# Kernel optimization log

Hardware: AMD Instinct MI355X
Metric: run time of the kernel (lower is better)

The kernel has to match this reference:

```python
import jax, jax.numpy as jnp
import numpy as np

D_MODEL, D_STATE, D_CONV, EXPAND = 1024, 16, 4, 2
D_INNER = EXPAND * D_MODEL
DT_RANK = max(16, D_MODEL // 16)
B_SZ, T_LEN = 2, 2048


def setup_inputs() -> dict:
    key = jax.random.key(0)
    ks = jax.random.split(key, 12)
    s = lambda fan: 1.0 / np.sqrt(fan)
    x = jax.random.normal(ks[0], (B_SZ, T_LEN, D_MODEL), jnp.float32)
    sigma2 = jax.random.uniform(ks[1], (B_SZ, T_LEN, 1), jnp.float32)
    W_in = jax.random.normal(ks[2], (D_MODEL, 2 * D_INNER), jnp.float32) * s(D_MODEL)
    conv_w = jax.random.normal(ks[3], (D_CONV, 1, D_INNER), jnp.float32) * s(D_CONV)
    conv_b = jax.random.normal(ks[4], (D_INNER,), jnp.float32) * 0.01
    W_xproj = jax.random.normal(ks[5], (D_INNER, 2 * D_STATE + DT_RANK), jnp.float32) * s(D_INNER)
    W_delta = jax.random.normal(ks[6], (D_MODEL, D_INNER), jnp.float32) * s(D_MODEL)
    b_delta = jax.random.normal(ks[7], (D_INNER,), jnp.float32) * 0.01
    A_log = jnp.log(jnp.tile(jnp.arange(1, D_STATE + 1, dtype=jnp.float32), (D_INNER, 1)))
    D_param = jnp.ones((D_INNER,), jnp.float32)
    W_out = jax.random.normal(ks[8], (D_INNER, D_MODEL), jnp.float32) * s(D_INNER)
    alpha = jnp.float32(1.0)
    return {"x": x, "sigma2": sigma2, "W_in": W_in, "conv_w": conv_w, "conv_b": conv_b,
            "W_xproj": W_xproj, "W_delta": W_delta, "b_delta": b_delta, "A_log": A_log,
            "D_param": D_param, "W_out": W_out, "alpha": alpha}


def _forward(x, sigma2, W_in, conv_w, conv_b, W_xproj, W_delta, b_delta, A_log, D_param, W_out, alpha):
    # in_proj and split
    xz = jnp.einsum('btd,de->bte', x, W_in)
    u, z = jnp.split(xz, 2, axis=-1)                      # (B,T,d_inner) each
    # causal depthwise conv1d (left pad d_conv-1, truncate to T)
    u = jax.lax.conv_general_dilated(
        u, conv_w, window_strides=(1,), padding=[(D_CONV - 1, 0)],
        dimension_numbers=('NHC', 'HIO', 'NHC'), feature_group_count=D_INNER) + conv_b
    u = jax.nn.silu(u)
    # x_proj -> B, C (delta_raw_proj branch is unused in custom-delta path)
    x_dbl = jnp.einsum('bti,ij->btj', u, W_xproj)
    Bp = x_dbl[..., :D_STATE]                              # (B,T,d_state)
    Cp = x_dbl[..., D_STATE:2 * D_STATE]                   # (B,T,d_state)
    # quality-gated custom delta
    delta_raw = jax.nn.softplus(jnp.einsum('btd,di->bti', x, W_delta) + b_delta)
    delta = delta_raw * jnp.exp(-alpha * sigma2)           # (B,T,d_inner)
    A = -jnp.exp(A_log)                                    # (d_inner,d_state)
    # discretize
    dA = jnp.exp(delta[..., None] * A)                     # (B,T,d_inner,d_state)
    dBu = delta[..., None] * Bp[:, :, None, :] * u[..., None]

    def step(h, inp):
        dA_t, dBu_t, c_t = inp                             # (B,di,ds),(B,di,ds),(B,ds)
        h = dA_t * h + dBu_t
        y_t = jnp.sum(h * c_t[:, None, :], axis=-1)        # (B,d_inner)
        return h, y_t

    h0 = jnp.zeros((x.shape[0], D_INNER, D_STATE), dtype=u.dtype)
    _, ys = jax.lax.scan(step, h0, (jnp.moveaxis(dA, 1, 0), jnp.moveaxis(dBu, 1, 0), jnp.moveaxis(Cp, 1, 0)))
    y = jnp.moveaxis(ys, 0, 1) + u * D_param               # (B,T,d_inner)
    y = y * jax.nn.silu(z)
    return jnp.einsum('bti,id->btd', y, W_out)


def reference(x, sigma2, W_in, conv_w, conv_b, W_xproj, W_delta, b_delta, A_log, D_param, W_out, alpha):
    return _forward(x, sigma2, W_in, conv_w, conv_b, W_xproj, W_delta, b_delta, A_log, D_param, W_out, alpha)
```

## Files before the change

### kernel.cpp

```cpp
#include <hip/hip_runtime.h>
#include <math.h>


constexpr int D_MODEL = 1024;
constexpr int D_STATE = 16;
constexpr int D_CONV  = 4;
constexpr int D_INNER = 2048;
constexpr int XPROJ_W = 96;
constexpr int B_SZ = 2, T_LEN = 2048;
constexpr int ROWS = B_SZ * T_LEN;
constexpr int NCHUNK = 64, CHUNK = T_LEN / NCHUNK;

typedef unsigned short ushort_t;
typedef __bf16 bf16x8 __attribute__((ext_vector_type(8)));
typedef float f32x4 __attribute__((ext_vector_type(4)));

__device__ __forceinline__ ushort_t f2bf(float f) {
  unsigned int u = __float_as_uint(f);
  u = (u + 0x7fffu + ((u >> 16) & 1u)) >> 16;
  return (ushort_t)u;
}
__device__ __forceinline__ float bf2f(ushort_t h) {
  return __uint_as_float(((unsigned int)h) << 16);
}

__device__ __forceinline__ void gload16(const void* g, void* l) {
  __builtin_amdgcn_global_load_lds(
      (const __attribute__((address_space(1))) void*)g,
      (__attribute__((address_space(3))) void*)l, 16, 0, 0);
}

__global__ __launch_bounds__(256)
void convert_all_kernel(const float* __restrict__ x,
                        const float* __restrict__ W_in,
                        const float* __restrict__ W_delta,
                        const float* __restrict__ W_out,
                        ushort_t* __restrict__ xb, ushort_t* __restrict__ WiT,
                        ushort_t* __restrict__ WdT, ushort_t* __restrict__ WoT)
{
  __shared__ float tile[32][33];
  const int blk = blockIdx.x;
  const int tid = threadIdx.x;
  if (blk < 4096) {
    const int i = blk * 256 + tid;
    const float4 v = ((const float4*)x)[i];
    ushort_t tmp[4] = {f2bf(v.x), f2bf(v.y), f2bf(v.z), f2bf(v.w)};
    ((uint2*)xb)[i] = *(const uint2*)tmp;
    return;
  }
  const float* in;
  ushort_t* out;
  int R, C, t;
  if (blk < 8192)      { in = W_in;    out = WiT; R = 1024; C = 4096; t = blk - 4096;  }
  else if (blk < 10240){ in = W_delta; out = WdT; R = 1024; C = 2048; t = blk - 8192;  }
  else                 { in = W_out;   out = WoT; R = 2048; C = 1024; t = blk - 10240; }
  const int tpr = C / 32;
  const int c0 = (t % tpr) * 32, r0 = (t / tpr) * 32;
  const int tx = tid & 31, ty = tid >> 5;
#pragma unroll
  for (int i = 0; i < 32; i += 8)
    tile[ty + i][tx] = in[(size_t)(r0 + ty + i) * C + c0 + tx];
  __syncthreads();
#pragma unroll
  for (int i = 0; i < 32; i += 8)
    out[(size_t)(c0 + ty + i) * R + r0 + tx] = f2bf(tile[tx][ty + i]);
}

template <int MODE, int BM>
__global__ __launch_bounds__(256)
void gemm_t(const ushort_t* __restrict__ A, const ushort_t* __restrict__ Bt,
            const int lda, const int ldb, const int KT,
            ushort_t* __restrict__ outB, float* __restrict__ outF,
            const float* __restrict__ bias, const float* __restrict__ sigma2,
            const float* __restrict__ alphap)
{
  constexpr int MREP = (BM == 32) ? 2 : 4;
  constexpr int NREP = (BM == 128) ? 4 : 2;
  constexpr int RT = BM + 128;
  constexpr int CH = RT / 32;

  __shared__ __align__(16) ushort_t As[BM * 64];
  __shared__ __align__(16) ushort_t Bs[128 * 64];
  const int tid = threadIdx.x;
  const int wave = tid >> 6, lane = tid & 63;
  const int lc = lane & 15, lr = lane >> 4;
  const int m0 = blockIdx.y * BM, n0 = blockIdx.x * 128;
  const int N = gridDim.x * 128;
  const int arow = (BM == 128) ? ((wave >> 1) * 64) : 0;
  const int bcol = (BM == 128) ? ((wave & 1) * 64) : (wave * 32);

  f32x4 acc[MREP][NREP];
#pragma unroll
  for (int i = 0; i < MREP; ++i)
#pragma unroll
    for (int j = 0; j < NREP; ++j) acc[i][j] = (f32x4)0.f;

  const int rlane = lane >> 3;
  const int clane = (lane & 7) * 8;

  for (int kt = 0; kt < KT; ++kt) {
    if (kt) __syncthreads();
    const int k0 = kt * 64;
#pragma unroll
    for (int i = 0; i < CH; ++i) {
      const int r0c = (wave * CH + i) * 8;
      if (r0c < BM) {
        gload16(A + (size_t)(m0 + r0c + rlane) * lda + k0 + clane,
                &As[r0c * 64]);
      } else {
        const int br = r0c - BM;
        gload16(Bt + (size_t)(n0 + br + rlane) * ldb + k0 + clane,
                &Bs[br * 64]);
      }
    }
    __syncthreads();
#pragma unroll
    for (int ks = 0; ks < 2; ++ks) {
      bf16x8 af[MREP], bfr[NREP];
#pragma unroll
      for (int mi = 0; mi < MREP; ++mi)
        af[mi] = *(const bf16x8*)
            &As[(arow + mi * 16 + lc) * 64 + ks * 32 + lr * 8];
#pragma unroll
      for (int ni = 0; ni < NREP; ++ni)
        bfr[ni] = *(const bf16x8*)
            &Bs[(bcol + ni * 16 + lc) * 64 + ks * 32 + lr * 8];
#pragma unroll
      for (int mi = 0; mi < MREP; ++mi)
#pragma unroll
        for (int ni = 0; ni < NREP; ++ni)
          acc[mi][ni] = __builtin_amdgcn_mfma_f32_16x16x32_bf16(
              af[mi], bfr[ni], acc[mi][ni], 0, 0, 0);
    }
  }

  const float alphaV = (MODE == 2) ? alphap[0] : 0.f;
#pragma unroll
  for (int mi = 0; mi < MREP; ++mi) {
    const int rowb = m0 + arow + mi * 16 + lr * 4;
#pragma unroll
    for (int ni = 0; ni < NREP; ++ni) {
      const int col = n0 + bcol + ni * 16 + lc;
      f32x4 v = acc[mi][ni];
      if (MODE == 0) {
#pragma unroll
        for (int r = 0; r < 4; ++r)
          outB[(size_t)(rowb + r) * N + col] = f2bf(v[r]);
      } else if (MODE == 2) {
        const float bv = bias[col];
#pragma unroll
        for (int r = 0; r < 4; ++r) {
          const float xv = v[r] + bv;
          const float sp = (xv > 20.f) ? xv : log1pf(__expf(xv));
          outB[(size_t)(rowb + r) * N + col] =
              f2bf(sp * __expf(-alphaV * sigma2[rowb + r]));
        }
      } else {
#pragma unroll
        for (int r = 0; r < 4; ++r)
          outF[(size_t)(rowb + r) * N + col] = v[r];
      }
    }
  }
}

__device__ __forceinline__ void decay_powers(float d, float (&dA)[16])
{
  const float q1 = __expf(-d);
  const float q2 = q1 * q1, q3 = q2 * q1, q4 = q2 * q2;
  const float q8 = q4 * q4, q12 = q8 * q4;
  dA[0] = q1;        dA[1] = q2;        dA[2] = q3;        dA[3] = q4;
  dA[4] = q4 * q1;   dA[5] = q4 * q2;   dA[6] = q4 * q3;   dA[7] = q8;
  dA[8] = q8 * q1;   dA[9] = q8 * q2;   dA[10] = q8 * q3;  dA[11] = q12;
  dA[12] = q12 * q1; dA[13] = q12 * q2; dA[14] = q12 * q3; dA[15] = q12 * q4;
}

__global__ __launch_bounds__(256)
void conv_xproj_kernel(const ushort_t* __restrict__ xzb,
                       const float* __restrict__ cw,
                       const float* __restrict__ cb,
                       const float* __restrict__ Wx,
                       ushort_t* __restrict__ u, float* __restrict__ BC)
{
  __shared__ float us[8][D_INNER];
  __shared__ float red[8][8][32];
  const int tid = threadIdx.x;
  const int b = blockIdx.y;
  const int t0 = blockIdx.x * 8;
  const int ch0 = tid * 8;

  float wtk[4][8], bs[8];
#pragma unroll
  for (int k = 0; k < 4; ++k) {
    float4 wa = *(const float4*)&cw[k * D_INNER + ch0];
    float4 wb = *(const float4*)&cw[k * D_INNER + ch0 + 4];
    wtk[k][0] = wa.x; wtk[k][1] = wa.y; wtk[k][2] = wa.z; wtk[k][3] = wa.w;
    wtk[k][4] = wb.x; wtk[k][5] = wb.y; wtk[k][6] = wb.z; wtk[k][7] = wb.w;
  }
  {
    float4 ba = *(const float4*)&cb[ch0];
    float4 bb = *(const float4*)&cb[ch0 + 4];
    bs[0] = ba.x; bs[1] = ba.y; bs[2] = ba.z; bs[3] = ba.w;
    bs[4] = bb.x; bs[5] = bb.y; bs[6] = bb.z; bs[7] = bb.w;
  }

#pragma unroll
  for (int r = 0; r < 8; ++r) {
    const int t = t0 + r;
    float acc[8];
#pragma unroll
    for (int j = 0; j < 8; ++j) acc[j] = bs[j];
#pragma unroll
    for (int k = 0; k < 4; ++k) {
      const int tt = t + k - 3;
      if (tt >= 0) {
        uint4 raw = *(const uint4*)
            &xzb[(size_t)(b * T_LEN + tt) * (2 * D_INNER) + ch0];
        const ushort_t* hp = (const ushort_t*)&raw;
#pragma unroll
        for (int j = 0; j < 8; ++j)
          acc[j] = fmaf(bf2f(hp[j]), wtk[k][j], acc[j]);
      }
    }
    ushort_t ub[8];
#pragma unroll
    for (int j = 0; j < 8; ++j) {
      const float ss = acc[j] / (1.f + __expf(-acc[j]));
      us[r][ch0 + j] = ss;
      ub[j] = f2bf(ss);
    }
    *(uint4*)&u[(size_t)(b * T_LEN + t) * D_INNER + ch0] = *(const uint4*)ub;
  }
  __syncthreads();

  const int j = tid & 31, chunk = tid >> 5;
  float p[8] = {0.f, 0.f, 0.f, 0.f, 0.f, 0.f, 0.f, 0.f};
  const float* WxC = Wx + j;
  for (int i = 0; i < 256; ++i) {
    const int k = chunk * 256 + i;
    const float w = WxC[(size_t)k * XPROJ_W];
#pragma unroll
    for (int r = 0; r < 8; ++r) p[r] = fmaf(us[r][k], w, p[r]);
  }
#pragma unroll
  for (int r = 0; r < 8; ++r) red[r][chunk][j] = p[r];
  __syncthreads();
  {
    const int r = tid >> 5, jj = tid & 31;
    float ssum = 0.f;
#pragma unroll
    for (int c = 0; c < 8; ++c) ssum += red[r][c][jj];
    BC[(size_t)(b * T_LEN + t0 + r) * 32 + jj] = ssum;
  }
}

__global__ __launch_bounds__(256)
void scan1_kernel(const ushort_t* __restrict__ delta,
                  const ushort_t* __restrict__ u,
                  const float* __restrict__ BC,
                  float* __restrict__ hEnd, float* __restrict__ sumD)
{
  const int c = blockIdx.x * 256 + threadIdx.x;
  const int b = blockIdx.y;
  const int j = blockIdx.z;
  float h[D_STATE];
#pragma unroll
  for (int n = 0; n < D_STATE; ++n) h[n] = 0.f;
  float sd = 0.f;
  const int t0 = j * CHUNK;
  for (int t = t0; t < t0 + CHUNK; ++t) {
    const int row = b * T_LEN + t;
    const float d = bf2f(delta[(size_t)row * D_INNER + c]);
    const float uu = bf2f(u[(size_t)row * D_INNER + c]);
    sd += d;
    const float du = d * uu;
    float dA[16];
    decay_powers(d, dA);
    const float4* bp4 = (const float4*)&BC[(size_t)row * 32];
    float4 b0 = bp4[0], b1 = bp4[1], b2 = bp4[2], b3 = bp4[3];
    const float bp[16] = {b0.x, b0.y, b0.z, b0.w, b1.x, b1.y, b1.z, b1.w,
                          b2.x, b2.y, b2.z, b2.w, b3.x, b3.y, b3.z, b3.w};
#pragma unroll
    for (int n = 0; n < D_STATE; ++n)
      h[n] = fmaf(dA[n], h[n], du * bp[n]);
  }
  const size_t base = ((size_t)b * D_INNER + c) * NCHUNK + j;
#pragma unroll
  for (int n = 0; n < D_STATE; ++n) hEnd[base * 16 + n] = h[n];
  sumD[base] = sd;
}

__global__ __launch_bounds__(256)
void scan2_kernel(float* __restrict__ hEnd, const float* __restrict__ sumD)
{
  const int idx = blockIdx.x * 256 + threadIdx.x;
  const int n = idx & 15;
  const int c = (idx >> 4) & (D_INNER - 1);
  const int b = idx >> 15;
  const float an = -(float)(n + 1);
  float H = 0.f;
  for (int j = 0; j < NCHUNK; ++j) {
    const size_t base = ((size_t)b * D_INNER + c) * NCHUNK + j;
    const float he = hEnd[base * 16 + n];
    const float sd = sumD[base];
    hEnd[base * 16 + n] = H;
    H = fmaf(__expf(an * sd), H, he);
  }
}

__global__ __launch_bounds__(256)
void scan3_kernel(const ushort_t* __restrict__ delta,
                  const ushort_t* __restrict__ u,
                  const float* __restrict__ BC,
                  const float* __restrict__ hStart,
                  const ushort_t* __restrict__ xzb,
                  const float* __restrict__ Dp, ushort_t* __restrict__ yb)
{
  const int c = blockIdx.x * 256 + threadIdx.x;
  const int b = blockIdx.y;
  const int j = blockIdx.z;
  float h[D_STATE];
  const size_t base = ((size_t)b * D_INNER + c) * NCHUNK + j;
#pragma unroll
  for (int n = 0; n < D_STATE; ++n) h[n] = hStart[base * 16 + n];
  const float dpc = Dp[c];
  const int t0 = j * CHUNK;
  for (int t = t0; t < t0 + CHUNK; ++t) {
    const int row = b * T_LEN + t;
    const float d = bf2f(delta[(size_t)row * D_INNER + c]);
    const float uu = bf2f(u[(size_t)row * D_INNER + c]);
    const float du = d * uu;
    float dA[16];
    decay_powers(d, dA);
    const float4* bc4 = (const float4*)&BC[(size_t)row * 32];
    float4 b0 = bc4[0], b1 = bc4[1], b2 = bc4[2], b3 = bc4[3];
    float4 c0 = bc4[4], c1 = bc4[5], c2 = bc4[6], c3 = bc4[7];
    const float bp[16] = {b0.x, b0.y, b0.z, b0.w, b1.x, b1.y, b1.z, b1.w,
                          b2.x, b2.y, b2.z, b2.w, b3.x, b3.y, b3.z, b3.w};
    const float cp[16] = {c0.x, c0.y, c0.z, c0.w, c1.x, c1.y, c1.z, c1.w,
                          c2.x, c2.y, c2.z, c2.w, c3.x, c3.y, c3.z, c3.w};
    float y = 0.f;
#pragma unroll
    for (int n = 0; n < D_STATE; ++n) {
      h[n] = fmaf(dA[n], h[n], du * bp[n]);
      y = fmaf(h[n], cp[n], y);
    }
    y = fmaf(uu, dpc, y);
    const float z = bf2f(xzb[(size_t)row * (2 * D_INNER) + D_INNER + c]);
    y *= z / (1.f + __expf(-z));
    yb[(size_t)row * D_INNER + c] = f2bf(y);
  }
}

extern "C" void kernel_launch(void* const* d_in, const int* in_sizes, int n_in,
                              void* d_out, int out_size, void* d_ws,
                              size_t ws_size, hipStream_t stream)
{
  const float* x       = (const float*)d_in[0];
  const float* sigma2  = (const float*)d_in[1];
  const float* W_in    = (const float*)d_in[2];
  const float* conv_w  = (const float*)d_in[3];
  const float* conv_b  = (const float*)d_in[4];
  const float* W_xproj = (const float*)d_in[5];
  const float* W_delta = (const float*)d_in[6];
  const float* b_delta = (const float*)d_in[7];
  const float* D_param = (const float*)d_in[9];
  const float* W_out   = (const float*)d_in[10];
  const float* alpha   = (const float*)d_in[11];
  float* out = (float*)d_out;

  char* ws = (char*)d_ws;
  ushort_t* xzb  = (ushort_t*)(ws);
  ushort_t* u    = (ushort_t*)(ws + ((size_t)32  << 20));
  ushort_t* dyb  = (ushort_t*)(ws + ((size_t)48  << 20));
  float*    BC   = (float*)   (ws + ((size_t)64  << 20));
  float*    hEnd = (float*)   (ws + ((size_t)65  << 20));
  float*    sumD = (float*)   (ws + ((size_t)81  << 20));
  ushort_t* xb   = (ushort_t*)(ws + ((size_t)82  << 20));
  ushort_t* WiT  = (ushort_t*)(ws + ((size_t)90  << 20));
  ushort_t* WdT  = (ushort_t*)(ws + ((size_t)98  << 20));
  ushort_t* WoT  = (ushort_t*)(ws + ((size_t)102 << 20));
  ushort_t* yb   = (ushort_t*)(ws + ((size_t)106 << 20));

  convert_all_kernel<<<12288, 256, 0, stream>>>(x, W_in, W_delta, W_out, xb,
                                                WiT, WdT, WoT);
  gemm_t<0, 128><<<dim3(4096 / 128, ROWS / 128), 256, 0, stream>>>(
      xb, WiT, 1024, 1024, 16, xzb, nullptr, nullptr, nullptr, nullptr);
  gemm_t<2, 64><<<dim3(2048 / 128, ROWS / 64), 256, 0, stream>>>(
      xb, WdT, 1024, 1024, 16, dyb, nullptr, b_delta, sigma2, alpha);
  conv_xproj_kernel<<<dim3(T_LEN / 8, B_SZ), 256, 0, stream>>>(
      xzb, conv_w, conv_b, W_xproj, u, BC);
  scan1_kernel<<<dim3(D_INNER / 256, B_SZ, NCHUNK), 256, 0, stream>>>(
      dyb, u, BC, hEnd, sumD);
  scan2_kernel<<<(B_SZ * D_INNER * D_STATE) / 256, 256, 0, stream>>>(hEnd,
                                                                     sumD);
  scan3_kernel<<<dim3(D_INNER / 256, B_SZ, NCHUNK), 256, 0, stream>>>(
      dyb, u, BC, hEnd, xzb, D_param, yb);
  gemm_t<1, 32><<<dim3(1024 / 128, ROWS / 32), 256, 0, stream>>>(
      yb, WoT, 2048, 2048, 32, nullptr, out, nullptr, nullptr, nullptr);
}
```

Baseline: 243.8 us.

## Merge independent stages into combined launches and halve scan chunk count

Splits weight conversion so the W_delta and W_out transposes run as extra blocks inside the in_proj GEMM launch. The conv+x_proj work and the delta GEMM now share one launch. This overlaps independent work and cuts launch count and tail idle time. The u tile in shared memory becomes bf16, which saves LDS but rounds the x_proj inputs. NCHUNK drops from 64 to 32, giving a longer sequential scan per chunk and less cross-chunk combine work.

```diff
diff --git a/kernel.cpp b/kernel.cpp
--- a/kernel.cpp
+++ b/kernel.cpp
@@ -9,7 +9,7 @@
 constexpr int XPROJ_W = 96;
 constexpr int B_SZ = 2, T_LEN = 2048;
 constexpr int ROWS = B_SZ * T_LEN;
-constexpr int NCHUNK = 64, CHUNK = T_LEN / NCHUNK;
+constexpr int NCHUNK = 32, CHUNK = T_LEN / NCHUNK;
 
 typedef unsigned short ushort_t;
 typedef __bf16 bf16x8 __attribute__((ext_vector_type(8)));
@@ -30,17 +30,30 @@
       (__attribute__((address_space(3))) void*)l, 16, 0, 0);
 }
 
-__global__ __launch_bounds__(256)
-void convert_all_kernel(const float* __restrict__ x,
-                        const float* __restrict__ W_in,
-                        const float* __restrict__ W_delta,
-                        const float* __restrict__ W_out,
-                        ushort_t* __restrict__ xb, ushort_t* __restrict__ WiT,
-                        ushort_t* __restrict__ WdT, ushort_t* __restrict__ WoT)
-{
-  __shared__ float tile[32][33];
-  const int blk = blockIdx.x;
-  const int tid = threadIdx.x;
+__device__ __forceinline__ void xpose_tile(const float* in, ushort_t* out,
+                                           int R, int C, int t, int tid,
+                                           char* smem)
+{
+  float (*tile)[33] = (float (*)[33])smem;
+  const int tpr = C / 32;
+  const int c0 = (t % tpr) * 32, r0 = (t / tpr) * 32;
+  const int tx = tid & 31, ty = tid >> 5;
+#pragma unroll
+  for (int i = 0; i < 32; i += 8)
+    tile[ty + i][tx] = in[(size_t)(r0 + ty + i) * C + c0 + tx];
+  __syncthreads();
+#pragma unroll
+  for (int i = 0; i < 32; i += 8)
+    out[(size_t)(c0 + ty + i) * R + r0 + tx] = f2bf(tile[tx][ty + i]);
+}
+
+__global__ __launch_bounds__(256)
+void convert_x_wi_kernel(const float* __restrict__ x,
+                         const float* __restrict__ W_in,
+                         ushort_t* __restrict__ xb, ushort_t* __restrict__ WiT)
+{
+  __shared__ __align__(16) char smem[4224];
+  const int blk = blockIdx.x, tid = threadIdx.x;
   if (blk < 4096) {
     const int i = blk * 256 + tid;
     const float4 v = ((const float4*)x)[i];
@@ -48,22 +61,241 @@
     ((uint2*)xb)[i] = *(const uint2*)tmp;
     return;
   }
-  const float* in;
-  ushort_t* out;
-  int R, C, t;
-  if (blk < 8192)      { in = W_in;    out = WiT; R = 1024; C = 4096; t = blk - 4096;  }
-  else if (blk < 10240){ in = W_delta; out = WdT; R = 1024; C = 2048; t = blk - 8192;  }
-  else                 { in = W_out;   out = WoT; R = 2048; C = 1024; t = blk - 10240; }
-  const int tpr = C / 32;
-  const int c0 = (t % tpr) * 32, r0 = (t / tpr) * 32;
-  const int tx = tid & 31, ty = tid >> 5;
-#pragma unroll
-  for (int i = 0; i < 32; i += 8)
-    tile[ty + i][tx] = in[(size_t)(r0 + ty + i) * C + c0 + tx];
-  __syncthreads();
-#pragma unroll
-  for (int i = 0; i < 32; i += 8)
-    out[(size_t)(c0 + ty + i) * R + r0 + tx] = f2bf(tile[tx][ty + i]);
+  xpose_tile(W_in, WiT, 1024, 4096, blk - 4096, tid, smem);
+}
+
+__global__ __launch_bounds__(256)
+void gemm1_xpose_kernel(const ushort_t* __restrict__ A,
+                        const ushort_t* __restrict__ Bt,
+                        ushort_t* __restrict__ outB,
+                        const float* __restrict__ W_delta,
+                        const float* __restrict__ W_out,
+                        ushort_t* __restrict__ WdT, ushort_t* __restrict__ WoT)
+{
+  __shared__ __align__(16) char smem[32768];
+  const int bid = blockIdx.x, tid = threadIdx.x;
+  if (bid >= 1024) {
+    int t = bid - 1024;
+    if (t < 2048) xpose_tile(W_delta, WdT, 1024, 2048, t, tid, smem);
+    else          xpose_tile(W_out,   WoT, 2048, 1024, t - 2048, tid, smem);
+    return;
+  }
+  ushort_t* As = (ushort_t*)smem;
+  ushort_t* Bs = (ushort_t*)(smem + 16384);
+  const int wave = tid >> 6, lane = tid & 63;
+  const int lc = lane & 15, lr = lane >> 4;
+  const int m0 = (bid >> 5) * 128, n0 = (bid & 31) * 128;
+  const int arow = (wave >> 1) * 64, bcol = (wave & 1) * 64;
+  const int rlane = lane >> 3, clane = (lane & 7) * 8;
+
+  f32x4 acc[4][4];
+#pragma unroll
+  for (int i = 0; i < 4; ++i)
+#pragma unroll
+    for (int j = 0; j < 4; ++j) acc[i][j] = (f32x4)0.f;
+
+  for (int kt = 0; kt < 16; ++kt) {
+    if (kt) __syncthreads();
+    const int k0 = kt * 64;
+#pragma unroll
+    for (int i = 0; i < 8; ++i) {
+      const int r0c = (wave * 8 + i) * 8;
+      if (r0c < 128)
+        gload16(A + (size_t)(m0 + r0c + rlane) * 1024 + k0 + clane,
+                &As[r0c * 64]);
+      else
+        gload16(Bt + (size_t)(n0 + r0c - 128 + rlane) * 1024 + k0 + clane,
+                &Bs[(r0c - 128) * 64]);
+    }
+    __syncthreads();
+#pragma unroll
+    for (int ks = 0; ks < 2; ++ks) {
+      bf16x8 af[4], bfr[4];
+#pragma unroll
+      for (int mi = 0; mi < 4; ++mi)
+        af[mi] = *(const bf16x8*)
+            &As[(arow + mi * 16 + lc) * 64 + ks * 32 + lr * 8];
+#pragma unroll
+      for (int ni = 0; ni < 4; ++ni)
+        bfr[ni] = *(const bf16x8*)
+            &Bs[(bcol + ni * 16 + lc) * 64 + ks * 32 + lr * 8];
+#pragma unroll
+      for (int mi = 0; mi < 4; ++mi)
+#pragma unroll
+        for (int ni = 0; ni < 4; ++ni)
+          acc[mi][ni] = __builtin_amdgcn_mfma_f32_16x16x32_bf16(
+              af[mi], bfr[ni], acc[mi][ni], 0, 0, 0);
+    }
+  }
+#pragma unroll
+  for (int mi = 0; mi < 4; ++mi) {
+    const int rowb = m0 + arow + mi * 16 + lr * 4;
+#pragma unroll
+    for (int ni = 0; ni < 4; ++ni) {
+      const int col = n0 + bcol + ni * 16 + lc;
+      f32x4 v = acc[mi][ni];
+#pragma unroll
+      for (int r = 0; r < 4; ++r)
+        outB[(size_t)(rowb + r) * 4096 + col] = f2bf(v[r]);
+    }
+  }
+}
+
+__global__ __launch_bounds__(256)
+void conv_gemm2_kernel(const ushort_t* __restrict__ xzb,
+                       const float* __restrict__ cw,
+                       const float* __restrict__ cb,
+                       const float* __restrict__ Wx,
+                       ushort_t* __restrict__ u, float* __restrict__ BC,
+                       const ushort_t* __restrict__ A,
+                       const ushort_t* __restrict__ WdT,
+                       ushort_t* __restrict__ dyb,
+                       const float* __restrict__ bias,
+                       const float* __restrict__ sigma2,
+                       const float* __restrict__ alphap)
+{
+  __shared__ __align__(16) char smem[40960];
+  const int bid = blockIdx.x, tid = threadIdx.x;
+
+  if (bid < 512) {
+    ushort_t (*usb)[D_INNER] = (ushort_t (*)[D_INNER])smem;
+    float (*red)[8][32] = (float (*)[8][32])(smem + 32768);
+    const int b = bid & 1;
+    const int t0 = (bid >> 1) * 8;
+    const int ch0 = tid * 8;
+
+    float wtk[4][8], bsv[8];
+#pragma unroll
+    for (int k = 0; k < 4; ++k) {
+      float4 wa = *(const float4*)&cw[k * D_INNER + ch0];
+      float4 wb = *(const float4*)&cw[k * D_INNER + ch0 + 4];
+      wtk[k][0] = wa.x; wtk[k][1] = wa.y; wtk[k][2] = wa.z; wtk[k][3] = wa.w;
+      wtk[k][4] = wb.x; wtk[k][5] = wb.y; wtk[k][6] = wb.z; wtk[k][7] = wb.w;
+    }
+    {
+      float4 ba = *(const float4*)&cb[ch0];
+      float4 bb = *(const float4*)&cb[ch0 + 4];
+      bsv[0] = ba.x; bsv[1] = ba.y; bsv[2] = ba.z; bsv[3] = ba.w;
+      bsv[4] = bb.x; bsv[5] = bb.y; bsv[6] = bb.z; bsv[7] = bb.w;
+    }
+#pragma unroll
+    for (int r = 0; r < 8; ++r) {
+      const int t = t0 + r;
+      float acc[8];
+#pragma unroll
+      for (int j = 0; j < 8; ++j) acc[j] = bsv[j];
+#pragma unroll
+      for (int k = 0; k < 4; ++k) {
+        const int tt = t + k - 3;
+        if (tt >= 0) {
+          uint4 raw = *(const uint4*)
+              &xzb[(size_t)(b * T_LEN + tt) * (2 * D_INNER) + ch0];
+          const ushort_t* hp = (const ushort_t*)&raw;
+#pragma unroll
+          for (int j = 0; j < 8; ++j)
+            acc[j] = fmaf(bf2f(hp[j]), wtk[k][j], acc[j]);
+        }
+      }
+      ushort_t ub[8];
+#pragma unroll
+      for (int j = 0; j < 8; ++j) {
+        const float ss = acc[j] / (1.f + __expf(-acc[j]));
+        ub[j] = f2bf(ss);
+      }
+      *(uint4*)&usb[r][ch0] = *(const uint4*)ub;
+      *(uint4*)&u[(size_t)(b * T_LEN + t) * D_INNER + ch0] = *(const uint4*)ub;
+    }
+    __syncthreads();
+
+    const int j = tid & 31, chunk = tid >> 5;
+    float p[8] = {0.f, 0.f, 0.f, 0.f, 0.f, 0.f, 0.f, 0.f};
+    const float* WxC = Wx + j;
+    for (int i = 0; i < 256; ++i) {
+      const int k = chunk * 256 + i;
+      const float w = WxC[(size_t)k * XPROJ_W];
+#pragma unroll
+      for (int r = 0; r < 8; ++r)
+        p[r] = fmaf(bf2f(usb[r][k]), w, p[r]);
+    }
+#pragma unroll
+    for (int r = 0; r < 8; ++r) red[r][chunk][j] = p[r];
+    __syncthreads();
+    {
+      const int r = tid >> 5, jj = tid & 31;
+      float ssum = 0.f;
+#pragma unroll
+      for (int c = 0; c < 8; ++c) ssum += red[r][c][jj];
+      BC[(size_t)(b * T_LEN + t0 + r) * 32 + jj] = ssum;
+    }
+    return;
+  }
+
+  ushort_t* As = (ushort_t*)smem;
+  ushort_t* Bs = (ushort_t*)(smem + 8192);
+  const int gidx = bid - 512;
+  const int wave = tid >> 6, lane = tid & 63;
+  const int lc = lane & 15, lr = lane >> 4;
+  const int m0 = (gidx >> 4) * 64, n0 = (gidx & 15) * 128;
+  const int bcol = wave * 32;
+  const int rlane = lane >> 3, clane = (lane & 7) * 8;
+
+  f32x4 acc[4][2];
+#pragma unroll
+  for (int i = 0; i < 4; ++i)
+#pragma unroll
+    for (int j = 0; j < 2; ++j) acc[i][j] = (f32x4)0.f;
+
+  for (int kt = 0; kt < 16; ++kt) {
+    if (kt) __syncthreads();
+    const int k0 = kt * 64;
+#pragma unroll
+    for (int i = 0; i < 6; ++i) {
+      const int r0c = (wave * 6 + i) * 8;
+      if (r0c < 64)
+        gload16(A + (size_t)(m0 + r0c + rlane) * 1024 + k0 + clane,
+                &As[r0c * 64]);
+      else
+        gload16(WdT + (size_t)(n0 + r0c - 64 + rlane) * 1024 + k0 + clane,
+                &Bs[(r0c - 64) * 64]);
+    }
+    __syncthreads();
+#pragma unroll
+    for (int ks = 0; ks < 2; ++ks) {
+      bf16x8 af[4], bfr[2];
+#pragma unroll
+      for (int mi = 0; mi < 4; ++mi)
+        af[mi] = *(const bf16x8*)
+            &As[(mi * 16 + lc) * 64 + ks * 32 + lr * 8];
+#pragma unroll
+      for (int ni = 0; ni < 2; ++ni)
+        bfr[ni] = *(const bf16x8*)
+            &Bs[(bcol + ni * 16 + lc) * 64 + ks * 32 + lr * 8];
+#pragma unroll
+      for (int mi = 0; mi < 4; ++mi)
+#pragma unroll
+        for (int ni = 0; ni < 2; ++ni)
+          acc[mi][ni] = __builtin_amdgcn_mfma_f32_16x16x32_bf16(
+              af[mi], bfr[ni], acc[mi][ni], 0, 0, 0);
+    }
+  }
+  const float alphaV = alphap[0];
+#pragma unroll
+  for (int mi = 0; mi < 4; ++mi) {
+    const int rowb = m0 + mi * 16 + lr * 4;
+#pragma unroll
+    for (int ni = 0; ni < 2; ++ni) {
+      const int col = n0 + bcol + ni * 16 + lc;
+      const float bv = bias[col];
+      f32x4 v = acc[mi][ni];
+#pragma unroll
+      for (int r = 0; r < 4; ++r) {
+        const float xv = v[r] + bv;
+        const float sp = (xv > 20.f) ? xv : log1pf(__expf(xv));
+        dyb[(size_t)(rowb + r) * 2048 + col] =
+            f2bf(sp * __expf(-alphaV * sigma2[rowb + r]));
+      }
+    }
+  }
 }
 
 template <int MODE, int BM>
@@ -104,14 +336,12 @@
 #pragma unroll
     for (int i = 0; i < CH; ++i) {
       const int r0c = (wave * CH + i) * 8;
-      if (r0c < BM) {
+      if (r0c < BM)
         gload16(A + (size_t)(m0 + r0c + rlane) * lda + k0 + clane,
                 &As[r0c * 64]);
-      } else {
-        const int br = r0c - BM;
-        gload16(Bt + (size_t)(n0 + br + rlane) * ldb + k0 + clane,
-                &Bs[br * 64]);
-      }
+      else
+        gload16(Bt + (size_t)(n0 + r0c - BM + rlane) * ldb + k0 + clane,
+                &Bs[(r0c - BM) * 64]);
     }
     __syncthreads();
 #pragma unroll
@@ -134,7 +364,6 @@
     }
   }
 
-  const float alphaV = (MODE == 2) ? alphap[0] : 0.f;
 #pragma unroll
   for (int mi = 0; mi < MREP; ++mi) {
     const int rowb = m0 + arow + mi * 16 + lr * 4;
@@ -142,24 +371,9 @@
     for (int ni = 0; ni < NREP; ++ni) {
       const int col = n0 + bcol + ni * 16 + lc;
       f32x4 v = acc[mi][ni];
-      if (MODE == 0) {
-#pragma unroll
-        for (int r = 0; r < 4; ++r)
-          outB[(size_t)(rowb + r) * N + col] = f2bf(v[r]);
-      } else if (MODE == 2) {
-        const float bv = bias[col];
-#pragma unroll
-        for (int r = 0; r < 4; ++r) {
-          const float xv = v[r] + bv;
-          const float sp = (xv > 20.f) ? xv : log1pf(__expf(xv));
-          outB[(size_t)(rowb + r) * N + col] =
-              f2bf(sp * __expf(-alphaV * sigma2[rowb + r]));
-        }
-      } else {
-#pragma unroll
-        for (int r = 0; r < 4; ++r)
-          outF[(size_t)(rowb + r) * N + col] = v[r];
-      }
+#pragma unroll
+      for (int r = 0; r < 4; ++r)
+        outF[(size_t)(rowb + r) * N + col] = v[r];
     }
   }
 }
@@ -173,85 +387,6 @@
   dA[4] = q4 * q1;   dA[5] = q4 * q2;   dA[6] = q4 * q3;   dA[7] = q8;
   dA[8] = q8 * q1;   dA[9] = q8 * q2;   dA[10] = q8 * q3;  dA[11] = q12;
   dA[12] = q12 * q1; dA[13] = q12 * q2; dA[14] = q12 * q3; dA[15] = q12 * q4;
-}
-
-__global__ __launch_bounds__(256)
-void conv_xproj_kernel(const ushort_t* __restrict__ xzb,
-                       const float* __restrict__ cw,
-                       const float* __restrict__ cb,
-                       const float* __restrict__ Wx,
-                       ushort_t* __restrict__ u, float* __restrict__ BC)
-{
-  __shared__ float us[8][D_INNER];
-  __shared__ float red[8][8][32];
-  const int tid = threadIdx.x;
-  const int b = blockIdx.y;
-  const int t0 = blockIdx.x * 8;
-  const int ch0 = tid * 8;
-
-  float wtk[4][8], bs[8];
-#pragma unroll
-  for (int k = 0; k < 4; ++k) {
-    float4 wa = *(const float4*)&cw[k * D_INNER + ch0];
-    float4 wb = *(const float4*)&cw[k * D_INNER + ch0 + 4];
-    wtk[k][0] = wa.x; wtk[k][1] = wa.y; wtk[k][2] = wa.z; wtk[k][3] = wa.w;
-    wtk[k][4] = wb.x; wtk[k][5] = wb.y; wtk[k][6] = wb.z; wtk[k][7] = wb.w;
-  }
-  {
-    float4 ba = *(const float4*)&cb[ch0];
-    float4 bb = *(const float4*)&cb[ch0 + 4];
-    bs[0] = ba.x; bs[1] = ba.y; bs[2] = ba.z; bs[3] = ba.w;
-    bs[4] = bb.x; bs[5] = bb.y; bs[6] = bb.z; bs[7] = bb.w;
-  }
-
-#pragma unroll
-  for (int r = 0; r < 8; ++r) {
-    const int t = t0 + r;
-    float acc[8];
-#pragma unroll
-    for (int j = 0; j < 8; ++j) acc[j] = bs[j];
-#pragma unroll
-    for (int k = 0; k < 4; ++k) {
-      const int tt = t + k - 3;
-      if (tt >= 0) {
-        uint4 raw = *(const uint4*)
-            &xzb[(size_t)(b * T_LEN + tt) * (2 * D_INNER) + ch0];
-        const ushort_t* hp = (const ushort_t*)&raw;
-#pragma unroll
-        for (int j = 0; j < 8; ++j)
-          acc[j] = fmaf(bf2f(hp[j]), wtk[k][j], acc[j]);
-      }
-    }
-    ushort_t ub[8];
-#pragma unroll
-    for (int j = 0; j < 8; ++j) {
-      const float ss = acc[j] / (1.f + __expf(-acc[j]));
-      us[r][ch0 + j] = ss;
-      ub[j] = f2bf(ss);
-    }
-    *(uint4*)&u[(size_t)(b * T_LEN + t) * D_INNER + ch0] = *(const uint4*)ub;
-  }
-  __syncthreads();
-
-  const int j = tid & 31, chunk = tid >> 5;
-  float p[8] = {0.f, 0.f, 0.f, 0.f, 0.f, 0.f, 0.f, 0.f};
-  const float* WxC = Wx + j;
-  for (int i = 0; i < 256; ++i) {
-    const int k = chunk * 256 + i;
-    const float w = WxC[(size_t)k * XPROJ_W];
-#pragma unroll
-    for (int r = 0; r < 8; ++r) p[r] = fmaf(us[r][k], w, p[r]);
-  }
-#pragma unroll
-  for (int r = 0; r < 8; ++r) red[r][chunk][j] = p[r];
-  __syncthreads();
-  {
-    const int r = tid >> 5, jj = tid & 31;
-    float ssum = 0.f;
-#pragma unroll
-    for (int c = 0; c < 8; ++c) ssum += red[r][c][jj];
-    BC[(size_t)(b * T_LEN + t0 + r) * 32 + jj] = ssum;
-  }
 }
 
 __global__ __launch_bounds__(256)
@@ -375,21 +510,19 @@
   ushort_t* dyb  = (ushort_t*)(ws + ((size_t)48  << 20));
   float*    BC   = (float*)   (ws + ((size_t)64  << 20));
   float*    hEnd = (float*)   (ws + ((size_t)65  << 20));
-  float*    sumD = (float*)   (ws + ((size_t)81  << 20));
-  ushort_t* xb   = (ushort_t*)(ws + ((size_t)82  << 20));
-  ushort_t* WiT  = (ushort_t*)(ws + ((size_t)90  << 20));
-  ushort_t* WdT  = (ushort_t*)(ws + ((size_t)98  << 20));
-  ushort_t* WoT  = (ushort_t*)(ws + ((size_t)102 << 20));
-  ushort_t* yb   = (ushort_t*)(ws + ((size_t)106 << 20));
-
-  convert_all_kernel<<<12288, 256, 0, stream>>>(x, W_in, W_delta, W_out, xb,
-                                                WiT, WdT, WoT);
-  gemm_t<0, 128><<<dim3(4096 / 128, ROWS / 128), 256, 0, stream>>>(
-      xb, WiT, 1024, 1024, 16, xzb, nullptr, nullptr, nullptr, nullptr);
-  gemm_t<2, 64><<<dim3(2048 / 128, ROWS / 64), 256, 0, stream>>>(
-      xb, WdT, 1024, 1024, 16, dyb, nullptr, b_delta, sigma2, alpha);
-  conv_xproj_kernel<<<dim3(T_LEN / 8, B_SZ), 256, 0, stream>>>(
-      xzb, conv_w, conv_b, W_xproj, u, BC);
+  float*    sumD = (float*)   (ws + ((size_t)82  << 20));
+  ushort_t* xb   = (ushort_t*)(ws + ((size_t)84  << 20));
+  ushort_t* WiT  = (ushort_t*)(ws + ((size_t)92  << 20));
+  ushort_t* WdT  = (ushort_t*)(ws + ((size_t)100 << 20));
+  ushort_t* WoT  = (ushort_t*)(ws + ((size_t)104 << 20));
+  ushort_t* yb   = (ushort_t*)(ws + ((size_t)108 << 20));
+
+  convert_x_wi_kernel<<<8192, 256, 0, stream>>>(x, W_in, xb, WiT);
+  gemm1_xpose_kernel<<<5120, 256, 0, stream>>>(xb, WiT, xzb, W_delta, W_out,
+                                               WdT, WoT);
+  conv_gemm2_kernel<<<1536, 256, 0, stream>>>(xzb, conv_w, conv_b, W_xproj, u,
+                                              BC, xb, WdT, dyb, b_delta,
+                                              sigma2, alpha);
   scan1_kernel<<<dim3(D_INNER / 256, B_SZ, NCHUNK), 256, 0, stream>>>(
       dyb, u, BC, hEnd, sumD);
   scan2_kernel<<<(B_SZ * D_INNER * D_STATE) / 256, 256, 0, stream>>>(hEnd,
```

New measurement: 238.1 us. 2.3% less time.
